# Optimization experiments

Measured on AMD Instinct MI355X. Metric: run time of the kernel, lower is better.

Reference implementation:

```python
import jax, jax.numpy as jnp
import numpy as np

B, SRC, TGT = 1024, 50, 25
I, H = 69, 1024          # input_size = 54 dofs + 15 actions; rnn_size
T = SRC + TGT - 1        # 74 frames total


def gru_cell(x, h, w_ih, w_hh, b_ih, b_hh):
    # PyTorch GRUCell math
    gi = x @ w_ih.T + b_ih            # [B, 3H]
    gh = h @ w_hh.T + b_hh            # [B, 3H]
    i_r, i_z, i_n = jnp.split(gi, 3, axis=-1)
    h_r, h_z, h_n = jnp.split(gh, 3, axis=-1)
    r = jax.nn.sigmoid(i_r + h_r)
    z = jax.nn.sigmoid(i_z + h_z)
    n = jnp.tanh(i_n + r * h_n)
    return (1.0 - z) * n + z * h


def setup_inputs() -> dict:
    key = jax.random.key(0)
    ks = jax.random.split(key, 10)
    s_ih = 1.0 / np.sqrt(H)
    return {
        "encoder_inputs": jax.random.normal(ks[0], (B, SRC, I), jnp.float32),
        "decoder_output": jax.random.normal(ks[1], (B, TGT - 1, I), jnp.float32),
        "w_ih": jax.random.uniform(ks[2], (3 * H, I), jnp.float32, -s_ih, s_ih),
        "w_hh": jax.random.uniform(ks[3], (3 * H, H), jnp.float32, -s_ih, s_ih),
        "b_ih": jax.random.uniform(ks[4], (3 * H,), jnp.float32, -s_ih, s_ih),
        "b_hh": jax.random.uniform(ks[5], (3 * H,), jnp.float32, -s_ih, s_ih),
        "fc1_w": jax.random.uniform(ks[6], (I, H), jnp.float32, -s_ih, s_ih),
        "fc1_b": jax.random.uniform(ks[7], (I,), jnp.float32, -s_ih, s_ih),
        "fc2_w": jax.random.uniform(ks[8], (1, I * T), jnp.float32, -0.01, 0.01),
        "fc2_b": jax.random.uniform(ks[9], (1,), jnp.float32, -0.01, 0.01),
    }


def reference(encoder_inputs, decoder_output, w_ih, w_hh, b_ih, b_hh,
              fc1_w, fc1_b, fc2_w, fc2_b):
    # Dropout is identity in eval mode; faithful deterministic reference.
    all_frame = jnp.concatenate([encoder_inputs, decoder_output], axis=1)  # [B,T,I]
    frames = jnp.transpose(all_frame, (1, 0, 2))                           # [T,B,I]
    batch = encoder_inputs.shape[0]
    state0 = jnp.zeros((batch, H), jnp.float32)

    # Encoding pass: GRU over all T frames
    def step1(h, x):
        return gru_cell(x, h, w_ih, w_hh, b_ih, b_hh), None
    state, _ = jax.lax.scan(step1, state0, frames)

    inp0 = frames[0]
    state = gru_cell(inp0, state, w_ih, w_hh, b_ih, b_hh)
    out0 = inp0 + state @ fc1_w.T + fc1_b

    def step2(carry, _):
        h, prev = carry
        h2 = gru_cell(prev, h, w_ih, w_hh, b_ih, b_hh)
        out = prev + h2 @ fc1_w.T + fc1_b
        return (h2, out), out
    _, rest = jax.lax.scan(step2, (state, out0), None, length=T - 1)

    outputs = jnp.concatenate([out0[None], rest], axis=0)   # [T,B,I]
    base = jnp.transpose(outputs, (1, 0, 2)).reshape(batch, -1)  # [B, T*I]
    logit = base @ fc2_w.T + fc2_b                           # [B,1]
    return jax.nn.sigmoid(logit)
```

## Files before the change

kernel.cpp:

```cpp
#include <hip/hip_runtime.h>
#include <hip/hip_bf16.h>

#define Bsz  1024
#define Hsz  1024
#define Isz  69
#define Tn   74
#define KP   1152
#define XP   128
#define XPF  80
#define XLP  84

typedef short  short8 __attribute__((ext_vector_type(8)));
typedef float  f32x4  __attribute__((ext_vector_type(4)));
using ushort = unsigned short;

__device__ __forceinline__ ushort f2bf(float f) {
    unsigned u = __float_as_uint(f);
    return (ushort)((u + 0x7fffu + ((u >> 16) & 1u)) >> 16);
}

__device__ __forceinline__ void gld_lds16(const void* g, void* l) {
    __builtin_amdgcn_global_load_lds(
        (const __attribute__((address_space(1))) unsigned int*)g,
        (__attribute__((address_space(3))) unsigned int*)l, 16, 0, 0);
}

__global__ void init_k(float* __restrict__ hf, ushort* __restrict__ hbf,
                       float* __restrict__ logit, const float* __restrict__ fc2_b) {
    unsigned gid = blockIdx.x * 256 + threadIdx.x;
    if (gid < 1024u * 1024u) { hf[gid] = 0.f; hbf[gid] = 0; }
    if (gid < 1024u) logit[gid] = fc2_b[0];
}

__global__ void pack_w(const float* __restrict__ w_ih, const float* __restrict__ w_hh,
                       const float* __restrict__ fc1_w,
                       ushort* __restrict__ wpack, ushort* __restrict__ w1p) {
    unsigned gid = blockIdx.x * 256 + threadIdx.x;
    const unsigned WN4 = 3072u * 288u;
    if (gid < WN4) {
        unsigned row = gid / 288u, c4 = (gid % 288u) * 4u;
        ushort4 o; ushort* po = (ushort*)&o;
#pragma unroll
        for (int e = 0; e < 4; ++e) {
            unsigned k = c4 + e; float v = 0.f;
            if (k < 1024u)       v = w_hh[(size_t)row * 1024u + k];
            else if (k < 1093u)  v = w_ih[(size_t)row * 69u + (k - 1024u)];
            po[e] = f2bf(v);
        }
        *(ushort4*)(wpack + (size_t)row * KP + c4) = o;
    } else if (gid < WN4 + 20480u) {
        unsigned g2 = gid - WN4;
        unsigned i = g2 / 256u, c4 = (g2 % 256u) * 4u;
        ushort4 o; ushort* po = (ushort*)&o;
#pragma unroll
        for (int e = 0; e < 4; ++e)
            po[e] = (i < 69u) ? f2bf(fc1_w[(size_t)i * 1024u + c4 + e]) : (ushort)0;
        *(ushort4*)(w1p + (size_t)i * 1024u + c4) = o;
    }
}

__global__ void pack_f(const float* __restrict__ enc, const float* __restrict__ dec,
                       ushort* __restrict__ frames, float* __restrict__ x0f) {
    unsigned gid = blockIdx.x * 256 + threadIdx.x;
    const unsigned NF4 = 74u * 1024u * 32u;
    if (gid < NF4) {
        unsigned c4 = (gid & 31u) * 4u;
        unsigned b  = (gid >> 5) & 1023u;
        unsigned tf = gid >> 15;
        ushort4 o; ushort* po = (ushort*)&o;
#pragma unroll
        for (int e = 0; e < 4; ++e) {
            unsigned i = c4 + e; float v = 0.f;
            if (i < 69u)
                v = (tf < 50u) ? enc[((size_t)b * 50u + tf) * 69u + i]
                               : dec[((size_t)b * 24u + (tf - 50u)) * 69u + i];
            po[e] = f2bf(v);
        }
        *(ushort4*)(frames + (size_t)tf * 1024u * XP + (size_t)b * XP + c4) = o;
    } else if (gid < NF4 + 81920u) {
        unsigned g2 = gid - NF4;
        unsigned b = g2 / 80u, i = g2 % 80u;
        x0f[g2] = (i < 69u) ? enc[(size_t)b * 50u * 69u + i] : 0.f;
    }
}

__launch_bounds__(512, 2)
__global__ void gru_fused(
    const ushort* __restrict__ hbf, const float* __restrict__ hf,
    const ushort* __restrict__ xframe, const float* __restrict__ xprevG,
    const ushort* __restrict__ wpack, const ushort* __restrict__ w1p,
    const float* __restrict__ b_ih, const float* __restrict__ b_hh,
    const float* __restrict__ fc1_b, const float* __restrict__ fc2_w,
    float* __restrict__ hf_out, ushort* __restrict__ hbf_out,
    float* __restrict__ xoutG, float* __restrict__ logitG, int d)
{
    __shared__ __align__(16) ushort ldsH[8 * 8192];
    __shared__ __align__(16) float  xLf[64 * XLP];

    const int t    = threadIdx.x;
    const int blk  = blockIdx.x;
    const int idx  = blk >> 3, xcd = blk & 7;
    const int bn   = xcd * 2 + (idx & 1);
    const int bm   = idx >> 1;
    const int wave = t >> 6, lane = t & 63;
    const int wk   = wave >> 2, wn = wave & 3;
    const int quad = lane >> 4, l16 = lane & 15;
    const int p_   = lane & 15, rl_ = lane >> 4;

#pragma unroll
    for (int c = 0; c < 8; ++c) {
#pragma unroll
        for (int i2 = 0; i2 < 2; ++i2) {
            const int srow = wave * 8 + i2 * 4 + rl_;
            const int cc   = p_ ^ (srow & 15);
            const ushort* g = hbf + (size_t)(bm * 64 + srow) * 1024 + c * 128 + cc * 8;
            gld_lds16(g, &ldsH[c * 8192 + (wave * 8 + i2 * 4) * 128]);
        }
    }

    const ushort* bp0 = wpack + (size_t)(bn * 64 + wn * 16 + l16) * KP + quad * 8 + wk * 64;
    const ushort* bp1 = bp0 + (size_t)1024 * KP;
    const ushort* bp2 = bp0 + (size_t)2048 * KP;
    short8 bq[8][3];
#pragma unroll
    for (int q = 0; q < 8; ++q) {
        bq[q][0] = *(const short8*)(bp0 + (q >> 1) * 128 + (q & 1) * 32);
        bq[q][1] = *(const short8*)(bp1 + (q >> 1) * 128 + (q & 1) * 32);
        bq[q][2] = *(const short8*)(bp2 + (q >> 1) * 128 + (q & 1) * 32);
    }

    float xp[4][4];
    if (d >= 1 && wave < 5) {
        const int j = wave * 16 + l16;
#pragma unroll
        for (int fm = 0; fm < 4; ++fm)
#pragma unroll
            for (int r = 0; r < 4; ++r)
                xp[fm][r] = xprevG[(size_t)(bm * 64 + fm * 16 + quad * 4 + r) * XPF + j];
    }
    __syncthreads();

    f32x4 accR[4], accZ[4], accNH[4], accNI[4];
#pragma unroll
    for (int i = 0; i < 4; ++i) {
        accR[i]  = (f32x4){0.f,0.f,0.f,0.f}; accZ[i]  = (f32x4){0.f,0.f,0.f,0.f};
        accNH[i] = (f32x4){0.f,0.f,0.f,0.f}; accNI[i] = (f32x4){0.f,0.f,0.f,0.f};
    }

#define MFMA_BF16 __builtin_amdgcn_mfma_f32_16x16x32_bf16
#pragma unroll
    for (int q = 0; q < 16; ++q) {
        const int c  = q >> 1, kk = q & 1;
        const int g  = (wk * 2 + kk) * 4 + quad;
        const ushort* ab = &ldsH[c * 8192];
        const int pos = (g ^ l16) * 8;
        short8 a0 = *(const short8*)(ab + ( 0 + l16) * 128 + pos);
        short8 a1 = *(const short8*)(ab + (16 + l16) * 128 + pos);
        short8 a2 = *(const short8*)(ab + (32 + l16) * 128 + pos);
        short8 a3 = *(const short8*)(ab + (48 + l16) * 128 + pos);
        short8 b0 = bq[q & 7][0], b1v = bq[q & 7][1], b2v = bq[q & 7][2];
        if (q < 10) {
            const int qc = (q + 8) >> 1, qk = (q + 8) & 1;
            bq[q & 7][0] = *(const short8*)(bp0 + qc * 128 + qk * 32);
            bq[q & 7][1] = *(const short8*)(bp1 + qc * 128 + qk * 32);
            bq[q & 7][2] = *(const short8*)(bp2 + qc * 128 + qk * 32);
        }
        accR[0] = MFMA_BF16(a0, b0, accR[0],0,0,0);
        accZ[0] = MFMA_BF16(a0, b1v, accZ[0],0,0,0);
        accNH[0]= MFMA_BF16(a0, b2v, accNH[0],0,0,0);
        accR[1] = MFMA_BF16(a1, b0, accR[1],0,0,0);
        accZ[1] = MFMA_BF16(a1, b1v, accZ[1],0,0,0);
        accNH[1]= MFMA_BF16(a1, b2v, accNH[1],0,0,0);
        accR[2] = MFMA_BF16(a2, b0, accR[2],0,0,0);
        accZ[2] = MFMA_BF16(a2, b1v, accZ[2],0,0,0);
        accNH[2]= MFMA_BF16(a2, b2v, accNH[2],0,0,0);
        accR[3] = MFMA_BF16(a3, b0, accR[3],0,0,0);
        accZ[3] = MFMA_BF16(a3, b1v, accZ[3],0,0,0);
        accNH[3]= MFMA_BF16(a3, b2v, accNH[3],0,0,0);
    }

    if (d >= 1 && wave < 5) {
        const int j = wave * 16 + l16;
        const ushort* bfp = w1p + (size_t)j * 1024 + quad * 8;
        f32x4 facc[4];
#pragma unroll
        for (int i = 0; i < 4; ++i) facc[i] = (f32x4){0.f,0.f,0.f,0.f};
#pragma unroll
        for (int c = 0; c < 8; ++c) {
#pragma unroll
            for (int q4 = 0; q4 < 4; ++q4) {
                short8 bb = *(const short8*)(bfp + c * 128 + q4 * 32);
#pragma unroll
                for (int fm = 0; fm < 4; ++fm) {
                    const int row = fm * 16 + l16;
                    short8 aa = *(const short8*)(&ldsH[c * 8192 + row * 128 + (((q4 * 4 + quad) ^ l16) * 8)]);
                    facc[fm] = MFMA_BF16(aa, bb, facc[fm],0,0,0);
                }
            }
        }
        const float b1f = (j < Isz) ? fc1_b[j] : 0.f;
#pragma unroll
        for (int fm = 0; fm < 4; ++fm)
#pragma unroll
            for (int r = 0; r < 4; ++r) {
                const int m = fm * 16 + quad * 4 + r;
                xLf[m * XLP + j] = (j < Isz) ? (xp[fm][r] + facc[fm][r] + b1f) : 0.f;
            }
    }
    __syncthreads();

    if (d >= 1 && bn == 0) {
        for (int i = t; i < 64 * XPF; i += 512) {
            const int r = i / XPF, c2 = i % XPF;
            xoutG[(size_t)(bm * 64 + r) * XPF + c2] = xLf[r * XLP + c2];
        }
    }

    short8 xf_[4][2];
    if (d < 1) {
#pragma unroll
        for (int kk = 0; kk < 2; ++kk) {
            const int gg = (wk * 2 + kk) * 4 + quad;
#pragma unroll
            for (int mt = 0; mt < 4; ++mt)
                xf_[mt][kk] = *(const short8*)(xframe + (size_t)(bm * 64 + mt * 16 + l16) * XP + gg * 8);
        }
    } else {
#pragma unroll
        for (int kk = 0; kk < 2; ++kk) {
            const int gg = (wk * 2 + kk) * 4 + quad;
#pragma unroll
            for (int mt = 0; mt < 4; ++mt) {
                short8 a = (short8){0,0,0,0,0,0,0,0};
                if (gg < 10) {
                    const float* p = &xLf[(mt * 16 + l16) * XLP + gg * 8];
                    f32x4 v0 = *(const f32x4*)p;
                    f32x4 v1 = *(const f32x4*)(p + 4);
                    union { short8 s; ushort u[8]; } uu;
                    uu.u[0] = f2bf(v0[0]); uu.u[1] = f2bf(v0[1]);
                    uu.u[2] = f2bf(v0[2]); uu.u[3] = f2bf(v0[3]);
                    uu.u[4] = f2bf(v1[0]); uu.u[5] = f2bf(v1[1]);
                    uu.u[6] = f2bf(v1[2]); uu.u[7] = f2bf(v1[3]);
                    a = uu.s;
                }
                xf_[mt][kk] = a;
            }
        }
    }
#pragma unroll
    for (int kk = 0; kk < 2; ++kk) {
        short8 b0 = bq[kk][0], b1v = bq[kk][1], b2v = bq[kk][2];
        accR[0] = MFMA_BF16(xf_[0][kk], b0, accR[0],0,0,0);
        accZ[0] = MFMA_BF16(xf_[0][kk], b1v, accZ[0],0,0,0);
        accNI[0]= MFMA_BF16(xf_[0][kk], b2v, accNI[0],0,0,0);
        accR[1] = MFMA_BF16(xf_[1][kk], b0, accR[1],0,0,0);
        accZ[1] = MFMA_BF16(xf_[1][kk], b1v, accZ[1],0,0,0);
        accNI[1]= MFMA_BF16(xf_[1][kk], b2v, accNI[1],0,0,0);
        accR[2] = MFMA_BF16(xf_[2][kk], b0, accR[2],0,0,0);
        accZ[2] = MFMA_BF16(xf_[2][kk], b1v, accZ[2],0,0,0);
        accNI[2]= MFMA_BF16(xf_[2][kk], b2v, accNI[2],0,0,0);
        accR[3] = MFMA_BF16(xf_[3][kk], b0, accR[3],0,0,0);
        accZ[3] = MFMA_BF16(xf_[3][kk], b1v, accZ[3],0,0,0);
        accNI[3]= MFMA_BF16(xf_[3][kk], b2v, accNI[3],0,0,0);
    }

    f32x4* exch = (f32x4*)ldsH;
    const int slot = wn * 64 + lane;
    {
        const int mtb = wk ? 0 : 2;
        f32x4* w = exch + wk * 2048;
#pragma unroll
        for (int i = 0; i < 2; ++i) {
            const int mt = mtb + i;
            w[(i * 4 + 0) * 256 + slot] = accR[mt];
            w[(i * 4 + 1) * 256 + slot] = accZ[mt];
            w[(i * 4 + 2) * 256 + slot] = accNH[mt];
            w[(i * 4 + 3) * 256 + slot] = accNI[mt];
        }
    }
    const int jcol = bn * 64 + wn * 16 + l16;
    const int mto  = wk * 2;
    float hp[2][4];
#pragma unroll
    for (int i = 0; i < 2; ++i)
#pragma unroll
        for (int r = 0; r < 4; ++r)
            hp[i][r] = hf[(size_t)(bm * 64 + (mto + i) * 16 + quad * 4 + r) * 1024 + jcol];
    __syncthreads();

    {
        const f32x4* rd = exch + (wk ^ 1) * 2048;
        const float bir = b_ih[jcol],        bhr = b_hh[jcol];
        const float biz = b_ih[1024 + jcol], bhz = b_hh[1024 + jcol];
        const float bin_= b_ih[2048 + jcol], bhn = b_hh[2048 + jcol];
#pragma unroll
        for (int i = 0; i < 2; ++i) {
            const int mt = mto + i;
            f32x4 aR = accR[mt] + rd[(i * 4 + 0) * 256 + slot];
            f32x4 aZ = accZ[mt] + rd[(i * 4 + 1) * 256 + slot];
            f32x4 aH = accNH[mt]+ rd[(i * 4 + 2) * 256 + slot];
            f32x4 aI = accNI[mt]+ rd[(i * 4 + 3) * 256 + slot];
#pragma unroll
            for (int r = 0; r < 4; ++r) {
                const int m = bm * 64 + mt * 16 + quad * 4 + r;
                float gr = aR[r] + bir + bhr;
                float gz = aZ[r] + biz + bhz;
                float rg = 1.f / (1.f + __expf(-gr));
                float zg = 1.f / (1.f + __expf(-gz));
                float nx = aI[r] + bin_ + rg * (aH[r] + bhn);
                nx = fminf(30.f, fmaxf(-30.f, nx));
                float e  = __expf(-2.f * nx);
                float ng = (1.f - e) / (1.f + e);
                float hn = (1.f - zg) * ng + zg * hp[i][r];
                hf_out[(size_t)m * 1024 + jcol]  = hn;
                hbf_out[(size_t)m * 1024 + jcol] = f2bf(hn);
            }
        }
    }

    if (d >= 1 && bn == 0 && wave == 5) {
        const int row = lane;
        float lp = 0.f;
        for (int c2 = 0; c2 < Isz; ++c2)
            lp += fc2_w[(size_t)(d - 1) * Isz + c2] * xLf[row * XLP + c2];
        logitG[bm * 64 + row] += lp;
    }
#undef MFMA_BF16
}

__launch_bounds__(512)
__global__ void tail_k(const ushort* __restrict__ hbf, const float* __restrict__ xprevG,
                       const ushort* __restrict__ w1p, const float* __restrict__ fc1_b,
                       const float* __restrict__ fc2_w, const float* __restrict__ logitG,
                       float* __restrict__ outp)
{
    __shared__ __align__(16) ushort ldsH[8 * 8192];
    __shared__ __align__(16) float  xLf[64 * XLP];
    const int t    = threadIdx.x;
    const int bm   = blockIdx.x;
    const int wave = t >> 6, lane = t & 63;
    const int quad = lane >> 4, l16 = lane & 15;
    const int p_   = lane & 15, rl_ = lane >> 4;

#pragma unroll
    for (int c = 0; c < 8; ++c) {
#pragma unroll
        for (int i2 = 0; i2 < 2; ++i2) {
            const int srow = wave * 8 + i2 * 4 + rl_;
            const int cc   = p_ ^ (srow & 15);
            const ushort* g = hbf + (size_t)(bm * 64 + srow) * 1024 + c * 128 + cc * 8;
            gld_lds16(g, &ldsH[c * 8192 + (wave * 8 + i2 * 4) * 128]);
        }
    }
    float xp[4][4];
    if (wave < 5) {
        const int j = wave * 16 + l16;
#pragma unroll
        for (int fm = 0; fm < 4; ++fm)
#pragma unroll
            for (int r = 0; r < 4; ++r)
                xp[fm][r] = xprevG[(size_t)(bm * 64 + fm * 16 + quad * 4 + r) * XPF + j];
    }
    __syncthreads();
    if (wave < 5) {
        const int j = wave * 16 + l16;
        const ushort* bfp = w1p + (size_t)j * 1024 + quad * 8;
        f32x4 facc[4];
#pragma unroll
        for (int i = 0; i < 4; ++i) facc[i] = (f32x4){0.f,0.f,0.f,0.f};
#pragma unroll
        for (int c = 0; c < 8; ++c) {
#pragma unroll
            for (int q4 = 0; q4 < 4; ++q4) {
                short8 bb = *(const short8*)(bfp + c * 128 + q4 * 32);
#pragma unroll
                for (int fm = 0; fm < 4; ++fm) {
                    const int row = fm * 16 + l16;
                    short8 aa = *(const short8*)(&ldsH[c * 8192 + row * 128 + (((q4 * 4 + quad) ^ l16) * 8)]);
                    facc[fm] = __builtin_amdgcn_mfma_f32_16x16x32_bf16(aa, bb, facc[fm],0,0,0);
                }
            }
        }
        const float b1f = (j < Isz) ? fc1_b[j] : 0.f;
#pragma unroll
        for (int fm = 0; fm < 4; ++fm)
#pragma unroll
            for (int r = 0; r < 4; ++r) {
                const int m = fm * 16 + quad * 4 + r;
                xLf[m * XLP + j] = (j < Isz) ? (xp[fm][r] + facc[fm][r] + b1f) : 0.f;
            }
    }
    __syncthreads();
    if (t < 64) {
        float lp = 0.f;
        for (int c2 = 0; c2 < Isz; ++c2)
            lp += fc2_w[(size_t)73 * Isz + c2] * xLf[t * XLP + c2];
        outp[bm * 64 + t] = 1.f / (1.f + __expf(-(logitG[bm * 64 + t] + lp)));
    }
}

extern "C" void kernel_launch(void* const* d_in, const int* in_sizes, int n_in,
                              void* d_out, int out_size, void* d_ws, size_t ws_size,
                              hipStream_t stream)
{
    const float* enc   = (const float*)d_in[0];
    const float* dec   = (const float*)d_in[1];
    const float* w_ih  = (const float*)d_in[2];
    const float* w_hh  = (const float*)d_in[3];
    const float* b_ih  = (const float*)d_in[4];
    const float* b_hh  = (const float*)d_in[5];
    const float* fc1_w = (const float*)d_in[6];
    const float* fc1_b = (const float*)d_in[7];
    const float* fc2_w = (const float*)d_in[8];
    const float* fc2_b = (const float*)d_in[9];
    float* out = (float*)d_out;

    char* ws = (char*)d_ws;
    size_t off = 0;
    auto alloc = [&](size_t bytes) -> void* {
        void* p = ws + off; off += (bytes + 255) & ~(size_t)255; return p;
    };
    ushort* wpack  = (ushort*)alloc((size_t)3072 * KP * 2);
    ushort* w1p    = (ushort*)alloc((size_t)80 * 1024 * 2);
    ushort* frames = (ushort*)alloc((size_t)Tn * 1024 * XP * 2);
    float*  x0f    = (float*) alloc((size_t)1024 * XPF * 4);
    float*  hfA    = (float*) alloc((size_t)1024 * 1024 * 4);
    float*  hfB    = (float*) alloc((size_t)1024 * 1024 * 4);
    ushort* hbfA   = (ushort*)alloc((size_t)1024 * 1024 * 2);
    ushort* hbfB   = (ushort*)alloc((size_t)1024 * 1024 * 2);
    float*  xGA    = (float*) alloc((size_t)1024 * XPF * 4);
    float*  xGB    = (float*) alloc((size_t)1024 * XPF * 4);
    float*  logit  = (float*) alloc((size_t)1024 * 4);

    init_k<<<4096, 256, 0, stream>>>(hfA, hbfA, logit, fc2_b);
    pack_w<<<3536, 256, 0, stream>>>(w_ih, w_hh, fc1_w, wpack, w1p);
    pack_f<<<9792, 256, 0, stream>>>(enc, dec, frames, x0f);

    float*  hf_c = hfA;  float*  hf_n = hfB;
    ushort* hb_c = hbfA; ushort* hb_n = hbfB;

    for (int tt = 0; tt < Tn + 1; ++tt) {
        const ushort* xfr = frames + (size_t)(tt < Tn ? tt : 0) * 1024 * XP;
        gru_fused<<<256, 512, 0, stream>>>(hb_c, hf_c, xfr, x0f, wpack, w1p,
                                           b_ih, b_hh, fc1_b, fc2_w,
                                           hf_n, hb_n, xGA, logit, 0);
        { float*  tf = hf_c; hf_c = hf_n; hf_n = tf; }
        { ushort* tb = hb_c; hb_c = hb_n; hb_n = tb; }
    }
    for (int d = 1; d < Tn; ++d) {
        const float* xin  = (d == 1) ? x0f : ((d & 1) ? xGB : xGA);
        float*       xout = (d & 1) ? xGA : xGB;
        gru_fused<<<256, 512, 0, stream>>>(hb_c, hf_c, frames, xin, wpack, w1p,
                                           b_ih, b_hh, fc1_b, fc2_w,
                                           hf_n, hb_n, xout, logit, d);
        { float*  tf = hf_c; hf_c = hf_n; hf_n = tf; }
        { ushort* tb = hb_c; hb_c = hb_n; hb_n = tb; }
    }
    tail_k<<<16, 512, 0, stream>>>(hb_c, xGA, w1p, fc1_b, fc2_w, logit, out);
}
```

Before: 4.189 ms.

## Drop fp32 hidden-state copy, keep only bf16 state; shrink weight prefetch ring

Removes the fp32 hidden-state buffers, so each step reads the previous h for the gate blend from the bf16 copy and writes only bf16. This cuts global traffic per step by roughly 6 MB of the roughly 9 MB of h reads and writes. The weight register prefetch drops from an 8-deep to a 2-deep ring, which frees VGPRs at the cost of less latency hiding. The encoder frame load is hoisted before the MFMA loop. The trade-off is precision: the recurrent state is now carried only in bf16 across 148 steps.

```diff
diff --git a/kernel.cpp b/kernel.cpp
--- a/kernel.cpp
+++ b/kernel.cpp
@@ -18,6 +18,9 @@
     unsigned u = __float_as_uint(f);
     return (ushort)((u + 0x7fffu + ((u >> 16) & 1u)) >> 16);
 }
+__device__ __forceinline__ float bf2f(ushort u) {
+    return __uint_as_float((unsigned)u << 16);
+}
 
 __device__ __forceinline__ void gld_lds16(const void* g, void* l) {
     __builtin_amdgcn_global_load_lds(
@@ -25,10 +28,10 @@
         (__attribute__((address_space(3))) unsigned int*)l, 16, 0, 0);
 }
 
-__global__ void init_k(float* __restrict__ hf, ushort* __restrict__ hbf,
-                       float* __restrict__ logit, const float* __restrict__ fc2_b) {
+__global__ void init_k(ushort* __restrict__ hbf, float* __restrict__ logit,
+                       const float* __restrict__ fc2_b) {
     unsigned gid = blockIdx.x * 256 + threadIdx.x;
-    if (gid < 1024u * 1024u) { hf[gid] = 0.f; hbf[gid] = 0; }
+    if (gid < 1024u * 1024u) hbf[gid] = 0;
     if (gid < 1024u) logit[gid] = fc2_b[0];
 }
 
@@ -86,12 +89,12 @@
 
 __launch_bounds__(512, 2)
 __global__ void gru_fused(
-    const ushort* __restrict__ hbf, const float* __restrict__ hf,
+    const ushort* __restrict__ hbf,
     const ushort* __restrict__ xframe, const float* __restrict__ xprevG,
     const ushort* __restrict__ wpack, const ushort* __restrict__ w1p,
     const float* __restrict__ b_ih, const float* __restrict__ b_hh,
     const float* __restrict__ fc1_b, const float* __restrict__ fc2_w,
-    float* __restrict__ hf_out, ushort* __restrict__ hbf_out,
+    ushort* __restrict__ hbf_out,
     float* __restrict__ xoutG, float* __restrict__ logitG, int d)
 {
     __shared__ __align__(16) ushort ldsH[8 * 8192];
@@ -121,16 +124,21 @@
     const ushort* bp0 = wpack + (size_t)(bn * 64 + wn * 16 + l16) * KP + quad * 8 + wk * 64;
     const ushort* bp1 = bp0 + (size_t)1024 * KP;
     const ushort* bp2 = bp0 + (size_t)2048 * KP;
-    short8 bq[8][3];
-#pragma unroll
-    for (int q = 0; q < 8; ++q) {
-        bq[q][0] = *(const short8*)(bp0 + (q >> 1) * 128 + (q & 1) * 32);
-        bq[q][1] = *(const short8*)(bp1 + (q >> 1) * 128 + (q & 1) * 32);
-        bq[q][2] = *(const short8*)(bp2 + (q >> 1) * 128 + (q & 1) * 32);
-    }
-
-    float xp[4][4];
-    if (d >= 1 && wave < 5) {
+    short8 bq[2][3];
+    bq[0][0] = *(const short8*)(bp0);      bq[0][1] = *(const short8*)(bp1);      bq[0][2] = *(const short8*)(bp2);
+    bq[1][0] = *(const short8*)(bp0 + 32); bq[1][1] = *(const short8*)(bp1 + 32); bq[1][2] = *(const short8*)(bp2 + 32);
+
+    short8 xf_[4][2];
+    float  xp[4][4];
+    if (d < 1) {
+#pragma unroll
+        for (int kk = 0; kk < 2; ++kk) {
+            const int gg = (wk * 2 + kk) * 4 + quad;
+#pragma unroll
+            for (int mt = 0; mt < 4; ++mt)
+                xf_[mt][kk] = *(const short8*)(xframe + (size_t)(bm * 64 + mt * 16 + l16) * XP + gg * 8);
+        }
+    } else if (wave < 5) {
         const int j = wave * 16 + l16;
 #pragma unroll
         for (int fm = 0; fm < 4; ++fm)
@@ -149,34 +157,33 @@
 
 #define MFMA_BF16 __builtin_amdgcn_mfma_f32_16x16x32_bf16
 #pragma unroll
-    for (int q = 0; q < 16; ++q) {
-        const int c  = q >> 1, kk = q & 1;
-        const int g  = (wk * 2 + kk) * 4 + quad;
-        const ushort* ab = &ldsH[c * 8192];
-        const int pos = (g ^ l16) * 8;
-        short8 a0 = *(const short8*)(ab + ( 0 + l16) * 128 + pos);
-        short8 a1 = *(const short8*)(ab + (16 + l16) * 128 + pos);
-        short8 a2 = *(const short8*)(ab + (32 + l16) * 128 + pos);
-        short8 a3 = *(const short8*)(ab + (48 + l16) * 128 + pos);
-        short8 b0 = bq[q & 7][0], b1v = bq[q & 7][1], b2v = bq[q & 7][2];
-        if (q < 10) {
-            const int qc = (q + 8) >> 1, qk = (q + 8) & 1;
-            bq[q & 7][0] = *(const short8*)(bp0 + qc * 128 + qk * 32);
-            bq[q & 7][1] = *(const short8*)(bp1 + qc * 128 + qk * 32);
-            bq[q & 7][2] = *(const short8*)(bp2 + qc * 128 + qk * 32);
-        }
-        accR[0] = MFMA_BF16(a0, b0, accR[0],0,0,0);
-        accZ[0] = MFMA_BF16(a0, b1v, accZ[0],0,0,0);
-        accNH[0]= MFMA_BF16(a0, b2v, accNH[0],0,0,0);
-        accR[1] = MFMA_BF16(a1, b0, accR[1],0,0,0);
-        accZ[1] = MFMA_BF16(a1, b1v, accZ[1],0,0,0);
-        accNH[1]= MFMA_BF16(a1, b2v, accNH[1],0,0,0);
-        accR[2] = MFMA_BF16(a2, b0, accR[2],0,0,0);
-        accZ[2] = MFMA_BF16(a2, b1v, accZ[2],0,0,0);
-        accNH[2]= MFMA_BF16(a2, b2v, accNH[2],0,0,0);
-        accR[3] = MFMA_BF16(a3, b0, accR[3],0,0,0);
-        accZ[3] = MFMA_BF16(a3, b1v, accZ[3],0,0,0);
-        accNH[3]= MFMA_BF16(a3, b2v, accNH[3],0,0,0);
+    for (int c = 0; c < 8; ++c) {
+#pragma unroll
+        for (int kk = 0; kk < 2; ++kk) {
+            const int g   = (wk * 2 + kk) * 4 + quad;
+            const ushort* ab = &ldsH[c * 8192];
+            const int pos = (g ^ l16) * 8;
+            short8 a0 = *(const short8*)(ab + ( 0 + l16) * 128 + pos);
+            short8 a1 = *(const short8*)(ab + (16 + l16) * 128 + pos);
+            short8 a2 = *(const short8*)(ab + (32 + l16) * 128 + pos);
+            short8 a3 = *(const short8*)(ab + (48 + l16) * 128 + pos);
+            short8 b0 = bq[kk][0], b1v = bq[kk][1], b2v = bq[kk][2];
+            bq[kk][0] = *(const short8*)(bp0 + (c + 1) * 128 + kk * 32);
+            bq[kk][1] = *(const short8*)(bp1 + (c + 1) * 128 + kk * 32);
+            bq[kk][2] = *(const short8*)(bp2 + (c + 1) * 128 + kk * 32);
+            accR[0] = MFMA_BF16(a0, b0, accR[0],0,0,0);
+            accZ[0] = MFMA_BF16(a0, b1v, accZ[0],0,0,0);
+            accNH[0]= MFMA_BF16(a0, b2v, accNH[0],0,0,0);
+            accR[1] = MFMA_BF16(a1, b0, accR[1],0,0,0);
+            accZ[1] = MFMA_BF16(a1, b1v, accZ[1],0,0,0);
+            accNH[1]= MFMA_BF16(a1, b2v, accNH[1],0,0,0);
+            accR[2] = MFMA_BF16(a2, b0, accR[2],0,0,0);
+            accZ[2] = MFMA_BF16(a2, b1v, accZ[2],0,0,0);
+            accNH[2]= MFMA_BF16(a2, b2v, accNH[2],0,0,0);
+            accR[3] = MFMA_BF16(a3, b0, accR[3],0,0,0);
+            accZ[3] = MFMA_BF16(a3, b1v, accZ[3],0,0,0);
+            accNH[3]= MFMA_BF16(a3, b2v, accNH[3],0,0,0);
+        }
     }
 
     if (d >= 1 && wave < 5) {
@@ -216,16 +223,7 @@
         }
     }
 
-    short8 xf_[4][2];
-    if (d < 1) {
-#pragma unroll
-        for (int kk = 0; kk < 2; ++kk) {
-            const int gg = (wk * 2 + kk) * 4 + quad;
-#pragma unroll
-            for (int mt = 0; mt < 4; ++mt)
-                xf_[mt][kk] = *(const short8*)(xframe + (size_t)(bm * 64 + mt * 16 + l16) * XP + gg * 8);
-        }
-    } else {
+    if (d >= 1) {
 #pragma unroll
         for (int kk = 0; kk < 2; ++kk) {
             const int gg = (wk * 2 + kk) * 4 + quad;
@@ -285,7 +283,7 @@
     for (int i = 0; i < 2; ++i)
 #pragma unroll
         for (int r = 0; r < 4; ++r)
-            hp[i][r] = hf[(size_t)(bm * 64 + (mto + i) * 16 + quad * 4 + r) * 1024 + jcol];
+            hp[i][r] = bf2f(hbf[(size_t)(bm * 64 + (mto + i) * 16 + quad * 4 + r) * 1024 + jcol]);
     __syncthreads();
 
     {
@@ -312,7 +310,6 @@
                 float e  = __expf(-2.f * nx);
                 float ng = (1.f - e) / (1.f + e);
                 float hn = (1.f - zg) * ng + zg * hp[i][r];
-                hf_out[(size_t)m * 1024 + jcol]  = hn;
                 hbf_out[(size_t)m * 1024 + jcol] = f2bf(hn);
             }
         }
@@ -424,36 +421,31 @@
     ushort* w1p    = (ushort*)alloc((size_t)80 * 1024 * 2);
     ushort* frames = (ushort*)alloc((size_t)Tn * 1024 * XP * 2);
     float*  x0f    = (float*) alloc((size_t)1024 * XPF * 4);
-    float*  hfA    = (float*) alloc((size_t)1024 * 1024 * 4);
-    float*  hfB    = (float*) alloc((size_t)1024 * 1024 * 4);
     ushort* hbfA   = (ushort*)alloc((size_t)1024 * 1024 * 2);
     ushort* hbfB   = (ushort*)alloc((size_t)1024 * 1024 * 2);
     float*  xGA    = (float*) alloc((size_t)1024 * XPF * 4);
     float*  xGB    = (float*) alloc((size_t)1024 * XPF * 4);
     float*  logit  = (float*) alloc((size_t)1024 * 4);
 
-    init_k<<<4096, 256, 0, stream>>>(hfA, hbfA, logit, fc2_b);
+    init_k<<<4096, 256, 0, stream>>>(hbfA, logit, fc2_b);
     pack_w<<<3536, 256, 0, stream>>>(w_ih, w_hh, fc1_w, wpack, w1p);
     pack_f<<<9792, 256, 0, stream>>>(enc, dec, frames, x0f);
 
-    float*  hf_c = hfA;  float*  hf_n = hfB;
     ushort* hb_c = hbfA; ushort* hb_n = hbfB;
 
     for (int tt = 0; tt < Tn + 1; ++tt) {
         const ushort* xfr = frames + (size_t)(tt < Tn ? tt : 0) * 1024 * XP;
-        gru_fused<<<256, 512, 0, stream>>>(hb_c, hf_c, xfr, x0f, wpack, w1p,
+        gru_fused<<<256, 512, 0, stream>>>(hb_c, xfr, x0f, wpack, w1p,
                                            b_ih, b_hh, fc1_b, fc2_w,
-                                           hf_n, hb_n, xGA, logit, 0);
-        { float*  tf = hf_c; hf_c = hf_n; hf_n = tf; }
+                                           hb_n, xGA, logit, 0);
         { ushort* tb = hb_c; hb_c = hb_n; hb_n = tb; }
     }
     for (int d = 1; d < Tn; ++d) {
         const float* xin  = (d == 1) ? x0f : ((d & 1) ? xGB : xGA);
         float*       xout = (d & 1) ? xGA : xGB;
-        gru_fused<<<256, 512, 0, stream>>>(hb_c, hf_c, frames, xin, wpack, w1p,
+        gru_fused<<<256, 512, 0, stream>>>(hb_c, frames, xin, wpack, w1p,
                                            b_ih, b_hh, fc1_b, fc2_w,
-                                           hf_n, hb_n, xout, logit, d);
-        { float*  tf = hf_c; hf_c = hf_n; hf_n = tf; }
+                                           hb_n, xout, logit, d);
         { ushort* tb = hb_c; hb_c = hb_n; hb_n = tb; }
     }
     tail_k<<<16, 512, 0, stream>>>(hb_c, xGA, w1p, fc1_b, fc2_w, logit, out);
```

After: 4.121 ms. Within noise of the previous version (-1.6%).
